# Kernel tuning notes

Hardware: AMD Instinct MI355X
Metric: run time of the kernel (lower is better)

The kernel has to match this reference:

```python
import jax, jax.numpy as jnp
import numpy as np

N_NODES = 50000
N_EDGES = 800000
NEG_SLOPE = 0.2


def _gat_layer(x, src, dst, W, a_src, a_dst, bias, heads, out_ch, concat, n_nodes):
    # x: [N, in_ch]; W: [in_ch, heads*out_ch]; a_src/a_dst: [heads, out_ch]
    h = (x @ W).reshape(n_nodes, heads, out_ch)          # [N, H, C]
    s_src = jnp.einsum('nhc,hc->nh', h, a_src)           # [N, H]
    s_dst = jnp.einsum('nhc,hc->nh', h, a_dst)           # [N, H]
    e = jax.nn.leaky_relu(s_src[src] + s_dst[dst], NEG_SLOPE)  # [E, H]
    # segment softmax over incoming edges of each destination node
    e_max = jax.ops.segment_max(e, dst, num_segments=n_nodes)   # [N, H]
    e_max = jnp.where(jnp.isfinite(e_max), e_max, 0.0)
    e_exp = jnp.exp(e - e_max[dst])                       # [E, H]
    denom = jax.ops.segment_sum(e_exp, dst, num_segments=n_nodes)  # [N, H]
    alpha = e_exp / denom[dst]                            # [E, H]
    msg = h[src] * alpha[:, :, None]                      # [E, H, C]
    out = jax.ops.segment_sum(msg, dst, num_segments=n_nodes)     # [N, H, C]
    if concat:
        out = out.reshape(n_nodes, heads * out_ch)
    else:
        out = out.mean(axis=1)
    return out + bias


def setup_inputs() -> dict:
    key = jax.random.key(0)
    ks = jax.random.split(key, 9)
    x = jax.random.normal(ks[0], (N_NODES, 128), dtype=jnp.float32)
    edge_index = jax.random.randint(ks[1], (2, N_EDGES), 0, N_NODES, dtype=jnp.int64)
    # glorot-ish scaled params
    W1 = jax.random.normal(ks[2], (128, 128), dtype=jnp.float32) * 0.1
    att_src1 = jax.random.normal(ks[3], (4, 32), dtype=jnp.float32) * 0.1
    att_dst1 = jax.random.normal(ks[4], (4, 32), dtype=jnp.float32) * 0.1
    bias1 = jnp.zeros((128,), dtype=jnp.float32)
    W2 = jax.random.normal(ks[5], (128, 64), dtype=jnp.float32) * 0.1
    att_src2 = jax.random.normal(ks[6], (1, 64), dtype=jnp.float32) * 0.1
    att_dst2 = jax.random.normal(ks[7], (1, 64), dtype=jnp.float32) * 0.1
    bias2 = jnp.zeros((64,), dtype=jnp.float32)
    return {"x": x, "edge_index": edge_index, "W1": W1, "att_src1": att_src1,
            "att_dst1": att_dst1, "bias1": bias1, "W2": W2, "att_src2": att_src2,
            "att_dst2": att_dst2, "bias2": bias2}


def reference(x, edge_index, W1, att_src1, att_dst1, bias1, W2, att_src2, att_dst2, bias2):
    n = x.shape[0]
    # PyG GATConv default add_self_loops=True
    loops = jnp.arange(n, dtype=edge_index.dtype)
    src = jnp.concatenate([edge_index[0], loops])
    dst = jnp.concatenate([edge_index[1], loops])
    h = _gat_layer(x, src, dst, W1, att_src1, att_dst1, bias1, 4, 32, True, n)
    h = jax.nn.relu(h)
    out = _gat_layer(h, src, dst, W2, att_src2, att_dst2, bias2, 1, 64, False, n)
    return out
```

## Files before the change

kernel.cpp:

```cpp
#include <hip/hip_runtime.h>
#include <hip/hip_bf16.h>


typedef __attribute__((ext_vector_type(8))) short bf16x8;
typedef __attribute__((ext_vector_type(4))) float f32x4;

#define BCHUNK 1024

__device__ __forceinline__ unsigned short f2bf(float f) {
  unsigned x = __float_as_uint(f);
  unsigned r = (x + 0x7fffu + ((x >> 16) & 1u)) >> 16;
  return (unsigned short)r;
}
__device__ __forceinline__ float bf2f(unsigned short u) {
  return __uint_as_float(((unsigned)u) << 16);
}
__device__ __forceinline__ float bflo(unsigned u) {
  return __uint_as_float(u << 16);
}
__device__ __forceinline__ float bfhi(unsigned u) {
  return __uint_as_float(u & 0xffff0000u);
}

__device__ __forceinline__ int lds_scan256(int v, int* s) {
  int tid = threadIdx.x;
  s[tid] = v;
  __syncthreads();
  for (int o = 1; o < 256; o <<= 1) {
    int t = (tid >= o) ? s[tid - o] : 0;
    __syncthreads();
    s[tid] += t;
    __syncthreads();
  }
  return s[tid];
}

__global__ __launch_bounds__(256) void b_count_cvt(
    const int* __restrict__ ei, int E, int N, int NBLK, int* __restrict__ cnt,
    const float* __restrict__ W1, const float* __restrict__ as1,
    const float* __restrict__ ad1, const float* __restrict__ W2,
    const float* __restrict__ as2, const float* __restrict__ ad2,
    unsigned short* __restrict__ W1t, unsigned short* __restrict__ W2t,
    unsigned short* __restrict__ wsb1, unsigned short* __restrict__ wsb2) {
  int tid = threadIdx.x;
  if ((int)blockIdx.x >= NBLK) {
    int i = ((int)blockIdx.x - NBLK) * 256 + tid;
    if (i < 16384) {
      int k = i >> 7, m = i & 127;
      W1t[m * 128 + k] = f2bf(W1[i]);
    } else if (i < 24576) {
      int j = i - 16384;
      int k = j / 64, m = j % 64;
      W2t[m * 128 + k] = f2bf(W2[j]);
    } else if (i < 26624) {
      int j = i - 24576;
      int m = j >> 7, k = j & 127;
      float acc = 0.f;
      if (m < 4) {
        for (int c = 0; c < 32; ++c) acc += W1[k * 128 + m * 32 + c] * as1[m * 32 + c];
      } else if (m < 8) {
        for (int c = 0; c < 32; ++c) acc += W1[k * 128 + (m - 4) * 32 + c] * ad1[(m - 4) * 32 + c];
      }
      wsb1[j] = f2bf(acc);
    } else if (i < 28672) {
      int j = i - 26624;
      int m = j >> 7, k = j & 127;
      float acc = 0.f;
      if (m == 0) {
        for (int c = 0; c < 64; ++c) acc += W2[k * 64 + c] * as2[c];
      } else if (m == 1) {
        for (int c = 0; c < 64; ++c) acc += W2[k * 64 + c] * ad2[c];
      }
      wsb2[j] = f2bf(acc);
    }
    return;
  }
  __shared__ int h[256];
  h[tid] = 0;
  __syncthreads();
  int ET = E + N;
  int base = blockIdx.x * BCHUNK;
  int lim = base + BCHUNK;
  if (lim > ET) lim = ET;
  for (int i = base + tid * 4; i < lim; i += 1024) {
    if (i + 3 < E && i + 4 <= lim) {
      int4 d4 = *(const int4*)(ei + E + i);
      atomicAdd(&h[d4.x >> 8], 1);
      atomicAdd(&h[d4.y >> 8], 1);
      atomicAdd(&h[d4.z >> 8], 1);
      atomicAdd(&h[d4.w >> 8], 1);
    } else {
      for (int k = 0; k < 4; ++k) {
        int idx = i + k;
        if (idx < lim) {
          int d = (idx < E) ? ei[E + idx] : (idx - E);
          atomicAdd(&h[d >> 8], 1);
        }
      }
    }
  }
  __syncthreads();
  cnt[(size_t)blockIdx.x * 256 + tid] = h[tid];
}

template <int AF32, int SC>
__global__ __launch_bounds__(256) void gemm_mfma(
    const void* __restrict__ Av, const unsigned short* __restrict__ Bt,
    const unsigned short* __restrict__ wsb, unsigned short* __restrict__ C,
    float* __restrict__ ssrc, float* __restrict__ sdst, int N, int M) {
  const int K = 128;
  int lane = threadIdx.x & 63;
  int wv = threadIdx.x >> 6;
  int row0 = blockIdx.x * 64 + wv * 16;
  if (row0 >= N) return;
  int r = lane & 15, quad = lane >> 4;

  bf16x8 a[4];
  if (AF32) {
    const float* ap = (const float*)Av + (size_t)(row0 + r) * K + quad * 8;
#pragma unroll
    for (int t = 0; t < 4; ++t) {
      float4 lo = *(const float4*)(ap + t * 32);
      float4 hi = *(const float4*)(ap + t * 32 + 4);
      a[t][0] = (short)f2bf(lo.x); a[t][1] = (short)f2bf(lo.y);
      a[t][2] = (short)f2bf(lo.z); a[t][3] = (short)f2bf(lo.w);
      a[t][4] = (short)f2bf(hi.x); a[t][5] = (short)f2bf(hi.y);
      a[t][6] = (short)f2bf(hi.z); a[t][7] = (short)f2bf(hi.w);
    }
  } else {
    const unsigned short* ap = (const unsigned short*)Av + (size_t)(row0 + r) * K + quad * 8;
#pragma unroll
    for (int t = 0; t < 4; ++t) a[t] = *(const bf16x8*)(ap + t * 32);
  }

  for (int c0 = 0; c0 < M; c0 += 16) {
    f32x4 acc = {0.f, 0.f, 0.f, 0.f};
    const unsigned short* bp = Bt + (size_t)(c0 + r) * K + quad * 8;
#pragma unroll
    for (int t = 0; t < 4; ++t) {
      bf16x8 b = *(const bf16x8*)(bp + t * 32);
      acc = __builtin_amdgcn_mfma_f32_16x16x32_bf16(a[t], b, acc, 0, 0, 0);
    }
    unsigned short* cp = C + (size_t)(row0 + quad * 4) * M + c0 + r;
#pragma unroll
    for (int i = 0; i < 4; ++i) cp[(size_t)i * M] = f2bf(acc[i]);
  }

  {
    f32x4 acc = {0.f, 0.f, 0.f, 0.f};
    const unsigned short* bp = wsb + r * 128 + quad * 8;
#pragma unroll
    for (int t = 0; t < 4; ++t) {
      bf16x8 b = *(const bf16x8*)(bp + t * 32);
      acc = __builtin_amdgcn_mfma_f32_16x16x32_bf16(a[t], b, acc, 0, 0, 0);
    }
    int row = row0 + quad * 4;
    if (r < SC) {
#pragma unroll
      for (int i = 0; i < 4; ++i) ssrc[(size_t)(row + i) * SC + r] = acc[i];
    } else if (r < 2 * SC) {
#pragma unroll
      for (int i = 0; i < 4; ++i) sdst[(size_t)(row + i) * SC + (r - SC)] = acc[i];
    }
  }
}


__global__ __launch_bounds__(256) void b_scan_bkt(const int* __restrict__ cnt, int NBLK,
                                                  int* __restrict__ blkoff,
                                                  int* __restrict__ bucketTotal) {
  __shared__ int s[256];
  int bucket = blockIdx.x, tid = threadIdx.x;
  int carry = 0;
  for (int base = 0; base < NBLK; base += 256) {
    int blk = base + tid;
    int v = (blk < NBLK) ? cnt[(size_t)blk * 256 + bucket] : 0;
    s[tid] = v;
    __syncthreads();
    for (int o = 1; o < 256; o <<= 1) {
      int t = (tid >= o) ? s[tid - o] : 0;
      __syncthreads();
      s[tid] += t;
      __syncthreads();
    }
    if (blk < NBLK) blkoff[(size_t)blk * 256 + bucket] = carry + s[tid] - v;
    carry += s[255];
    __syncthreads();
  }
  if (tid == 0) bucketTotal[bucket] = carry;
}

__global__ __launch_bounds__(256) void b_scatter(
    const int* __restrict__ ei, int E, int N,
    const int* __restrict__ bucketTotal, const int* __restrict__ blkoff,
    unsigned* __restrict__ bkt) {
  __shared__ int s[256];
  __shared__ int lcur[256];
  int tid = threadIdx.x;
  int tot = bucketTotal[tid];
  int incl = lds_scan256(tot, s);
  lcur[tid] = (incl - tot) + blkoff[(size_t)blockIdx.x * 256 + tid];
  __syncthreads();
  int ET = E + N;
  int base = blockIdx.x * BCHUNK;
  int lim = base + BCHUNK;
  if (lim > ET) lim = ET;
  for (int i = base + tid * 4; i < lim; i += 1024) {
    if (i + 3 < E && i + 4 <= lim) {
      int4 s4 = *(const int4*)(ei + i);
      int4 d4 = *(const int4*)(ei + E + i);
      int slot;
      slot = atomicAdd(&lcur[d4.x >> 8], 1); bkt[slot] = (unsigned)s4.x | ((unsigned)(d4.x & 255) << 16);
      slot = atomicAdd(&lcur[d4.y >> 8], 1); bkt[slot] = (unsigned)s4.y | ((unsigned)(d4.y & 255) << 16);
      slot = atomicAdd(&lcur[d4.z >> 8], 1); bkt[slot] = (unsigned)s4.z | ((unsigned)(d4.z & 255) << 16);
      slot = atomicAdd(&lcur[d4.w >> 8], 1); bkt[slot] = (unsigned)s4.w | ((unsigned)(d4.w & 255) << 16);
    } else {
      for (int k = 0; k < 4; ++k) {
        int idx = i + k;
        if (idx < lim) {
          int s_, d;
          if (idx < E) { s_ = ei[idx]; d = ei[E + idx]; }
          else { s_ = idx - E; d = s_; }
          int slot = atomicAdd(&lcur[d >> 8], 1);
          bkt[slot] = (unsigned)s_ | ((unsigned)(d & 255) << 16);
        }
      }
    }
  }
}

__global__ __launch_bounds__(256) void b_bucketsort(
    const unsigned* __restrict__ bkt, const int* __restrict__ bucketTotal,
    unsigned* __restrict__ csr4, int* __restrict__ rowptr, int N, int ET) {
  __shared__ int s[256];
  __shared__ int cnt[256];
  int b = blockIdx.x, tid = threadIdx.x;
  int tot = bucketTotal[tid];
  (void)lds_scan256(tot, s);
  int base = (b == 0) ? 0 : s[b - 1];
  int end = s[b];
  __syncthreads();
  cnt[tid] = 0;
  __syncthreads();
  for (int i = base + tid; i < end; i += 512) {
    unsigned p0 = bkt[i];
    int i1 = i + 256;
    unsigned p1 = (i1 < end) ? bkt[i1] : 0u;
    atomicAdd(&cnt[p0 >> 16], 1);
    if (i1 < end) atomicAdd(&cnt[p1 >> 16], 1);
  }
  __syncthreads();
  int v = cnt[tid];
  int incl = lds_scan256(v, s);
  int excl = incl - v;
  int node = (b << 8) + tid;
  if (node < N) rowptr[node] = base + excl;
  if (tid == 0 && b == gridDim.x - 1) rowptr[N] = ET;
  cnt[tid] = base + excl;
  __syncthreads();
  for (int i = base + tid; i < end; i += 512) {
    unsigned p0 = bkt[i];
    int i1 = i + 256;
    unsigned p1 = (i1 < end) ? bkt[i1] : 0u;
    int slot0 = atomicAdd(&cnt[p0 >> 16], 1);
    csr4[slot0] = p0;
    if (i1 < end) {
      int slot1 = atomicAdd(&cnt[p1 >> 16], 1);
      csr4[slot1] = p1;
    }
  }
}

template <int H, int C, int L, int OUT_BF16>
__global__ __launch_bounds__(256) void gat_aggr4(
    const int* __restrict__ rowptr, const unsigned* __restrict__ csr4,
    const float* __restrict__ ssrc, const float* __restrict__ sdst,
    const unsigned short* __restrict__ h, const float* __restrict__ bias,
    void* __restrict__ outv, int N) {
  const int HC = H * C;
  const int G = 64 / L;
  int lane = threadIdx.x & 63;
  int n = blockIdx.x * 4 + (threadIdx.x >> 6);
  if (n >= N) return;
  int l = lane & (L - 1);
  int g = lane / L;
  int c0 = l * 8;
  int hh = c0 / C;
  int beg = rowptr[n];
  int cnt = rowptr[n + 1] - beg;
  float sdn = sdst[(size_t)n * H + hh];
  float a0 = 0.f, a1 = 0.f, a2 = 0.f, a3 = 0.f;
  float a4 = 0.f, a5 = 0.f, a6 = 0.f, a7 = 0.f, ws = 0.f;

  int j = g;
  for (; j + G < cnt; j += 2 * G) {
    int i0 = beg + j, i1 = beg + j + G;
    int s0 = (int)(csr4[i0] & 0xFFFF);
    int s1 = (int)(csr4[i1] & 0xFFFF);
    float e0 = ssrc[(size_t)s0 * H + hh] + sdn;
    float e1 = ssrc[(size_t)s1 * H + hh] + sdn;
    e0 = e0 > 0.f ? e0 : 0.2f * e0;
    e1 = e1 > 0.f ? e1 : 0.2f * e1;
    float w0 = __expf(e0);
    float w1 = __expf(e1);
    uint4 u0 = *(const uint4*)(h + (size_t)s0 * HC + c0);
    uint4 u1 = *(const uint4*)(h + (size_t)s1 * HC + c0);
    a0 = fmaf(w0, bflo(u0.x), a0); a1 = fmaf(w0, bfhi(u0.x), a1);
    a2 = fmaf(w0, bflo(u0.y), a2); a3 = fmaf(w0, bfhi(u0.y), a3);
    a4 = fmaf(w0, bflo(u0.z), a4); a5 = fmaf(w0, bfhi(u0.z), a5);
    a6 = fmaf(w0, bflo(u0.w), a6); a7 = fmaf(w0, bfhi(u0.w), a7);
    a0 = fmaf(w1, bflo(u1.x), a0); a1 = fmaf(w1, bfhi(u1.x), a1);
    a2 = fmaf(w1, bflo(u1.y), a2); a3 = fmaf(w1, bfhi(u1.y), a3);
    a4 = fmaf(w1, bflo(u1.z), a4); a5 = fmaf(w1, bfhi(u1.z), a5);
    a6 = fmaf(w1, bflo(u1.w), a6); a7 = fmaf(w1, bfhi(u1.w), a7);
    ws += w0 + w1;
  }
  if (j < cnt) {
    int i0 = beg + j;
    int s0 = (int)(csr4[i0] & 0xFFFF);
    float e0 = ssrc[(size_t)s0 * H + hh] + sdn;
    e0 = e0 > 0.f ? e0 : 0.2f * e0;
    float w0 = __expf(e0);
    uint4 u0 = *(const uint4*)(h + (size_t)s0 * HC + c0);
    a0 = fmaf(w0, bflo(u0.x), a0); a1 = fmaf(w0, bfhi(u0.x), a1);
    a2 = fmaf(w0, bflo(u0.y), a2); a3 = fmaf(w0, bfhi(u0.y), a3);
    a4 = fmaf(w0, bflo(u0.z), a4); a5 = fmaf(w0, bfhi(u0.z), a5);
    a6 = fmaf(w0, bflo(u0.w), a6); a7 = fmaf(w0, bfhi(u0.w), a7);
    ws += w0;
  }
#pragma unroll
  for (int off = L; off < 64; off <<= 1) {
    a0 += __shfl_xor(a0, off, 64); a1 += __shfl_xor(a1, off, 64);
    a2 += __shfl_xor(a2, off, 64); a3 += __shfl_xor(a3, off, 64);
    a4 += __shfl_xor(a4, off, 64); a5 += __shfl_xor(a5, off, 64);
    a6 += __shfl_xor(a6, off, 64); a7 += __shfl_xor(a7, off, 64);
    ws += __shfl_xor(ws, off, 64);
  }
  if (lane < L) {
    float inv = 1.f / ws;
    float4 bA = *(const float4*)(bias + c0);
    float4 bB = *(const float4*)(bias + c0 + 4);
    float v0 = fmaf(a0, inv, bA.x), v1 = fmaf(a1, inv, bA.y);
    float v2 = fmaf(a2, inv, bA.z), v3 = fmaf(a3, inv, bA.w);
    float v4 = fmaf(a4, inv, bB.x), v5 = fmaf(a5, inv, bB.y);
    float v6 = fmaf(a6, inv, bB.z), v7 = fmaf(a7, inv, bB.w);
    if (OUT_BF16) {
      v0 = fmaxf(v0, 0.f); v1 = fmaxf(v1, 0.f);
      v2 = fmaxf(v2, 0.f); v3 = fmaxf(v3, 0.f);
      v4 = fmaxf(v4, 0.f); v5 = fmaxf(v5, 0.f);
      v6 = fmaxf(v6, 0.f); v7 = fmaxf(v7, 0.f);
      uint4 o;
      o.x = (unsigned)f2bf(v0) | ((unsigned)f2bf(v1) << 16);
      o.y = (unsigned)f2bf(v2) | ((unsigned)f2bf(v3) << 16);
      o.z = (unsigned)f2bf(v4) | ((unsigned)f2bf(v5) << 16);
      o.w = (unsigned)f2bf(v6) | ((unsigned)f2bf(v7) << 16);
      ((uint4*)outv)[(size_t)n * (HC / 8) + l] = o;
    } else {
      float* op = (float*)outv + (size_t)n * HC + c0;
      *(float4*)op = make_float4(v0, v1, v2, v3);
      *(float4*)(op + 4) = make_float4(v4, v5, v6, v7);
    }
  }
}

extern "C" void kernel_launch(void* const* d_in, const int* in_sizes, int n_in,
                              void* d_out, int out_size, void* d_ws, size_t ws_size,
                              hipStream_t stream) {
  const float* x   = (const float*)d_in[0];
  const int*   ei  = (const int*)d_in[1];
  const float* W1  = (const float*)d_in[2];
  const float* as1 = (const float*)d_in[3];
  const float* ad1 = (const float*)d_in[4];
  const float* b1  = (const float*)d_in[5];
  const float* W2  = (const float*)d_in[6];
  const float* as2 = (const float*)d_in[7];
  const float* ad2 = (const float*)d_in[8];
  const float* b2  = (const float*)d_in[9];

  const int N = in_sizes[0] / 128;
  const int E = in_sizes[1] / 2;
  const int ET = E + N;
  const int NBKT = (N + 255) >> 8;
  const int NBLK = (ET + BCHUNK - 1) / BCHUNK;

  char* pc = (char*)d_ws;
  auto alloc = [&](size_t bytes) -> void* {
    void* r = (void*)pc;
    pc += (bytes + 255) & ~(size_t)255;
    return r;
  };
  unsigned short* h1b   = (unsigned short*)alloc((size_t)N * 128 * 2);
  unsigned short* out1b = (unsigned short*)alloc((size_t)N * 128 * 2);
  unsigned short* W1t   = (unsigned short*)alloc(128 * 128 * 2);
  unsigned short* W2t   = (unsigned short*)alloc(64 * 128 * 2);
  unsigned short* wsb1  = (unsigned short*)alloc(16 * 128 * 2);
  unsigned short* wsb2  = (unsigned short*)alloc(16 * 128 * 2);
  float* ssrc1 = (float*)alloc((size_t)N * 4 * 4);
  float* sdst1 = (float*)alloc((size_t)N * 4 * 4);
  float* ssrc2 = (float*)alloc((size_t)N * 4);
  float* sdst2 = (float*)alloc((size_t)N * 4);
  int* rowptr      = (int*)alloc((size_t)(N + 1) * 4);
  int* cnt         = (int*)alloc((size_t)NBLK * 256 * 4);
  int* blkoff      = (int*)alloc((size_t)NBLK * 256 * 4);
  int* bucketTotal = (int*)alloc(256 * 4);
  unsigned* bkt  = (unsigned*)alloc((size_t)ET * 4);
  unsigned* csr4 = (unsigned*)alloc((size_t)ET * 4);
  unsigned short* h2b = h1b;

  dim3 blk(256);

  b_count_cvt<<<dim3(NBLK + 112), blk, 0, stream>>>(
      ei, E, N, NBLK, cnt, W1, as1, ad1, W2, as2, ad2, W1t, W2t, wsb1, wsb2);
  b_scan_bkt<<<dim3(256), blk, 0, stream>>>(cnt, NBLK, blkoff, bucketTotal);
  b_scatter<<<dim3(NBLK), blk, 0, stream>>>(ei, E, N, bucketTotal, blkoff, bkt);
  b_bucketsort<<<dim3(NBKT), blk, 0, stream>>>(bkt, bucketTotal, csr4, rowptr, N, ET);

  gemm_mfma<1, 4><<<dim3((N + 63) / 64), blk, 0, stream>>>(
      x, W1t, wsb1, h1b, ssrc1, sdst1, N, 128);
  gat_aggr4<4, 32, 16, 1><<<dim3((N + 3) / 4), blk, 0, stream>>>(
      rowptr, csr4, ssrc1, sdst1, h1b, b1, out1b, N);

  gemm_mfma<0, 1><<<dim3((N + 63) / 64), blk, 0, stream>>>(
      out1b, W2t, wsb2, h2b, ssrc2, sdst2, N, 64);
  gat_aggr4<1, 64, 8, 0><<<dim3((N + 3) / 4), blk, 0, stream>>>(
      rowptr, csr4, ssrc2, sdst2, h2b, b2, d_out, N);
}
```

Baseline: 212.4 us.

## Split layer-1 GEMM across CSR build kernels to overlap independent work

The layer-1 GEMM no longer runs as its own launch. Its row blocks are split into three parts and appended as extra blocks to the scan, scatter and bucket-sort kernels that build the CSR. This fills idle GPU capacity during the small, latency-bound sort phases and removes one kernel launch. The cost is heterogeneous blocks in each kernel, which can hurt occupancy and scheduling, and the split ratios are fixed heuristics.

```diff
diff --git a/kernel.cpp b/kernel.cpp
--- a/kernel.cpp
+++ b/kernel.cpp
@@ -104,15 +104,12 @@
 }
 
 template <int AF32, int SC>
-__global__ __launch_bounds__(256) void gemm_mfma(
+__device__ __forceinline__ void gemm_body(
     const void* __restrict__ Av, const unsigned short* __restrict__ Bt,
     const unsigned short* __restrict__ wsb, unsigned short* __restrict__ C,
-    float* __restrict__ ssrc, float* __restrict__ sdst, int N, int M) {
+    float* __restrict__ ssrc, float* __restrict__ sdst, int M, int row0) {
   const int K = 128;
   int lane = threadIdx.x & 63;
-  int wv = threadIdx.x >> 6;
-  int row0 = blockIdx.x * 64 + wv * 16;
-  if (row0 >= N) return;
   int r = lane & 15, quad = lane >> 4;
 
   bf16x8 a[4];
@@ -165,10 +162,20 @@
   }
 }
 
-
-__global__ __launch_bounds__(256) void b_scan_bkt(const int* __restrict__ cnt, int NBLK,
-                                                  int* __restrict__ blkoff,
-                                                  int* __restrict__ bucketTotal) {
+template <int AF32, int SC>
+__global__ __launch_bounds__(256) void gemm_mfma(
+    const void* __restrict__ Av, const unsigned short* __restrict__ Bt,
+    const unsigned short* __restrict__ wsb, unsigned short* __restrict__ C,
+    float* __restrict__ ssrc, float* __restrict__ sdst, int N, int M) {
+  int row0 = blockIdx.x * 64 + (threadIdx.x >> 6) * 16;
+  if (row0 >= N) return;
+  gemm_body<AF32, SC>(Av, Bt, wsb, C, ssrc, sdst, M, row0);
+}
+
+
+__device__ __forceinline__ void scan_body(const int* __restrict__ cnt, int NBLK,
+                                          int* __restrict__ blkoff,
+                                          int* __restrict__ bucketTotal) {
   __shared__ int s[256];
   int bucket = blockIdx.x, tid = threadIdx.x;
   int carry = 0;
@@ -190,7 +197,7 @@
   if (tid == 0) bucketTotal[bucket] = carry;
 }
 
-__global__ __launch_bounds__(256) void b_scatter(
+__device__ __forceinline__ void scatter_body(
     const int* __restrict__ ei, int E, int N,
     const int* __restrict__ bucketTotal, const int* __restrict__ blkoff,
     unsigned* __restrict__ bkt) {
@@ -229,9 +236,10 @@
   }
 }
 
-__global__ __launch_bounds__(256) void b_bucketsort(
+__device__ __forceinline__ void sort_body(
     const unsigned* __restrict__ bkt, const int* __restrict__ bucketTotal,
-    unsigned* __restrict__ csr4, int* __restrict__ rowptr, int N, int ET) {
+    unsigned* __restrict__ csr4, int* __restrict__ rowptr, int N, int ET,
+    int NBKT) {
   __shared__ int s[256];
   __shared__ int cnt[256];
   int b = blockIdx.x, tid = threadIdx.x;
@@ -255,7 +263,7 @@
   int excl = incl - v;
   int node = (b << 8) + tid;
   if (node < N) rowptr[node] = base + excl;
-  if (tid == 0 && b == gridDim.x - 1) rowptr[N] = ET;
+  if (tid == 0 && b == NBKT - 1) rowptr[N] = ET;
   cnt[tid] = base + excl;
   __syncthreads();
   for (int i = base + tid; i < end; i += 512) {
@@ -269,6 +277,53 @@
       csr4[slot1] = p1;
     }
   }
+}
+
+__global__ __launch_bounds__(256) void k_scan_gemm1(
+    const int* __restrict__ cnt, int NBLK, int* __restrict__ blkoff,
+    int* __restrict__ bucketTotal,
+    const float* __restrict__ x, const unsigned short* __restrict__ W1t,
+    const unsigned short* __restrict__ wsb1, unsigned short* __restrict__ h1b,
+    float* __restrict__ ssrc1, float* __restrict__ sdst1, int N, int rowBase) {
+  if ((int)blockIdx.x < 256) {
+    scan_body(cnt, NBLK, blkoff, bucketTotal);
+    return;
+  }
+  int row0 = rowBase + ((int)blockIdx.x - 256) * 64 + (threadIdx.x >> 6) * 16;
+  if (row0 >= N) return;
+  gemm_body<1, 4>(x, W1t, wsb1, h1b, ssrc1, sdst1, 128, row0);
+}
+
+__global__ __launch_bounds__(256) void k_scatter_gemm1(
+    const int* __restrict__ ei, int E, int Nn,
+    const int* __restrict__ bucketTotal, const int* __restrict__ blkoff,
+    unsigned* __restrict__ bkt, int NBLK,
+    const float* __restrict__ x, const unsigned short* __restrict__ W1t,
+    const unsigned short* __restrict__ wsb1, unsigned short* __restrict__ h1b,
+    float* __restrict__ ssrc1, float* __restrict__ sdst1, int rowBase) {
+  if ((int)blockIdx.x < NBLK) {
+    scatter_body(ei, E, Nn, bucketTotal, blkoff, bkt);
+    return;
+  }
+  int row0 = rowBase + ((int)blockIdx.x - NBLK) * 64 + (threadIdx.x >> 6) * 16;
+  if (row0 >= Nn) return;
+  gemm_body<1, 4>(x, W1t, wsb1, h1b, ssrc1, sdst1, 128, row0);
+}
+
+__global__ __launch_bounds__(256) void k_sort_gemm1(
+    const unsigned* __restrict__ bkt, const int* __restrict__ bucketTotal,
+    unsigned* __restrict__ csr4, int* __restrict__ rowptr, int Nn, int ET,
+    int NBKT,
+    const float* __restrict__ x, const unsigned short* __restrict__ W1t,
+    const unsigned short* __restrict__ wsb1, unsigned short* __restrict__ h1b,
+    float* __restrict__ ssrc1, float* __restrict__ sdst1, int rowBase) {
+  if ((int)blockIdx.x < NBKT) {
+    sort_body(bkt, bucketTotal, csr4, rowptr, Nn, ET, NBKT);
+    return;
+  }
+  int row0 = rowBase + ((int)blockIdx.x - NBKT) * 64 + (threadIdx.x >> 6) * 16;
+  if (row0 >= Nn) return;
+  gemm_body<1, 4>(x, W1t, wsb1, h1b, ssrc1, sdst1, 128, row0);
 }
 
 template <int H, int C, int L, int OUT_BF16>
@@ -409,14 +464,24 @@
 
   dim3 blk(256);
 
+  const int GB  = (N + 63) / 64;
+  const int GB1 = GB / 5;
+  const int GB2 = GB / 4;
+  const int GB3 = GB - GB1 - GB2;
+  const int rowBase2 = GB1 * 64;
+  const int rowBase3 = (GB1 + GB2) * 64;
+
   b_count_cvt<<<dim3(NBLK + 112), blk, 0, stream>>>(
       ei, E, N, NBLK, cnt, W1, as1, ad1, W2, as2, ad2, W1t, W2t, wsb1, wsb2);
-  b_scan_bkt<<<dim3(256), blk, 0, stream>>>(cnt, NBLK, blkoff, bucketTotal);
-  b_scatter<<<dim3(NBLK), blk, 0, stream>>>(ei, E, N, bucketTotal, blkoff, bkt);
-  b_bucketsort<<<dim3(NBKT), blk, 0, stream>>>(bkt, bucketTotal, csr4, rowptr, N, ET);
-
-  gemm_mfma<1, 4><<<dim3((N + 63) / 64), blk, 0, stream>>>(
-      x, W1t, wsb1, h1b, ssrc1, sdst1, N, 128);
+  k_scan_gemm1<<<dim3(256 + GB1), blk, 0, stream>>>(
+      cnt, NBLK, blkoff, bucketTotal, x, W1t, wsb1, h1b, ssrc1, sdst1, N, 0);
+  k_scatter_gemm1<<<dim3(NBLK + GB2), blk, 0, stream>>>(
+      ei, E, N, bucketTotal, blkoff, bkt, NBLK,
+      x, W1t, wsb1, h1b, ssrc1, sdst1, rowBase2);
+  k_sort_gemm1<<<dim3(NBKT + GB3), blk, 0, stream>>>(
+      bkt, bucketTotal, csr4, rowptr, N, ET, NBKT,
+      x, W1t, wsb1, h1b, ssrc1, sdst1, rowBase3);
+
   gat_aggr4<4, 32, 16, 1><<<dim3((N + 3) / 4), blk, 0, stream>>>(
       rowptr, csr4, ssrc1, sdst1, h1b, b1, out1b, N);
 
```

New measurement: 205.0 us. -3.5%, faster.
